# Kernel optimization log

Measured on AMD Instinct MI355X. Metric: run time of the kernel, lower is better.

The kernel has to match this reference:

```python
import jax, jax.numpy as jnp
import numpy as np

D_MODEL = 2048
N_HEADS = 16
HEAD_DIM = D_MODEL // N_HEADS
MLP_DIM = 4 * D_MODEL
RMS_EPS = 1e-6
MASK_VALUE = -1e9  # fp32 path in the original


def setup_inputs() -> dict:
    key = jax.random.key(0)
    ks = jax.random.split(key, 8)
    B, S = 2, 2048
    scale = 0.02
    return {
        "x": jax.random.normal(ks[0], (B, S, D_MODEL), dtype=jnp.float32),
        "attention_mask": jnp.ones((B, S), dtype=jnp.int32),
        "w_norm_attn": jnp.ones((D_MODEL,), dtype=jnp.float32),
        "wq": jax.random.normal(ks[1], (D_MODEL, D_MODEL), dtype=jnp.float32) * scale,
        "wk": jax.random.normal(ks[2], (D_MODEL, D_MODEL), dtype=jnp.float32) * scale,
        "wv": jax.random.normal(ks[3], (D_MODEL, D_MODEL), dtype=jnp.float32) * scale,
        "wo": jax.random.normal(ks[4], (D_MODEL, D_MODEL), dtype=jnp.float32) * scale,
        "w_norm_mlp": jnp.ones((D_MODEL,), dtype=jnp.float32),
        "w_up": jax.random.normal(ks[5], (MLP_DIM, D_MODEL), dtype=jnp.float32) * scale,
        "w_down": jax.random.normal(ks[6], (D_MODEL, MLP_DIM), dtype=jnp.float32) * scale,
    }


def _rmsnorm(x, w, eps=RMS_EPS):
    rms = jax.lax.rsqrt(jnp.mean(x * x, axis=-1, keepdims=True) + eps)
    return x * rms * w


def _split_heads(x):  # [B,S,D] -> [B,H,S,Dh]
    B, S, _ = x.shape
    return x.reshape(B, S, N_HEADS, HEAD_DIM).transpose(0, 2, 1, 3)


def reference(x, attention_mask, w_norm_attn, wq, wk, wv, wo, w_norm_mlp, w_up, w_down):
    B, S, _ = x.shape
    residual = x
    h = _rmsnorm(x, w_norm_attn)
    # nn.Linear(no bias): y = h @ W.T
    q = _split_heads(h @ wq.T)  # [B,H,S,Dh]
    k = _split_heads(h @ wk.T)
    v = _split_heads(h @ wv.T)

    scale = 1.0 / np.sqrt(HEAD_DIM)
    scores = jnp.einsum("bhqd,bhkd->bhqk", q, k) * scale  # [B,H,S,S]

    q_pos = jnp.arange(S)[:, None]
    k_pos = jnp.arange(S)[None, :]
    causal = k_pos <= q_pos  # [S,S]
    scores = jnp.where(causal[None, None], scores, MASK_VALUE)

    key_mask = attention_mask.astype(bool)  # [B,S]
    scores = jnp.where(key_mask[:, None, None, :], scores, MASK_VALUE)

    probs = jax.nn.softmax(scores.astype(jnp.float32), axis=-1).astype(q.dtype)
    probs = jnp.nan_to_num(probs, nan=0.0, posinf=0.0, neginf=0.0)

    att = jnp.einsum("bhqk,bhkd->bhqd", probs, v)  # [B,H,S,Dh]
    att = att.transpose(0, 2, 1, 3).reshape(B, S, D_MODEL)
    x = residual + att @ wo.T

    residual = x
    h = _rmsnorm(x, w_norm_mlp)
    h = jax.nn.gelu(h @ w_up.T, approximate=False)  # F.gelu default is exact erf
    x = residual + h @ w_down.T
    return x
```

## Files before the change

kernel.cpp:

```cpp
#include <hip/hip_runtime.h>

typedef unsigned short u16;
typedef __bf16 bf16x8 __attribute__((ext_vector_type(8)));
typedef float f32x4 __attribute__((ext_vector_type(4)));

#define SEQ 2048
#define DM 2048
#define NH 16
#define DHD 128
#define MLPD 8192
#define ATT_SCALE 0.08838834764831845f

__device__ __forceinline__ float bf2f(u16 u) {
  union { unsigned int i; float f; } c; c.i = ((unsigned int)u) << 16; return c.f;
}
__device__ __forceinline__ u16 f2bf(float f) {
  union { float f; unsigned int i; } c; c.f = f;
  unsigned int u = c.i;
  u += 0x7FFFu + ((u >> 16) & 1u);
  return (u16)(u >> 16);
}

__device__ __forceinline__ bool path_is_bf16(const unsigned* chk) {
  return chk[0] == 0x3F803F80u;
}

__device__ __forceinline__ void gl_lds16(const void* g, void* l) {
  __builtin_amdgcn_global_load_lds(
      (const __attribute__((address_space(1))) void*)g,
      (__attribute__((address_space(3))) void*)l, 16, 0, 0);
}

__global__ __launch_bounds__(256) void conv_w(const float* __restrict__ in,
                                              u16* __restrict__ out,
                                              const unsigned* __restrict__ chk) {
  if (path_is_bf16(chk)) return;
  size_t i = ((size_t)blockIdx.x * 256 + threadIdx.x) * 8;
  float4 a = *(const float4*)(in + i), b = *(const float4*)(in + i + 4);
  union { uint4 u; u16 s[8]; } o;
  o.s[0]=f2bf(a.x); o.s[1]=f2bf(a.y); o.s[2]=f2bf(a.z); o.s[3]=f2bf(a.w);
  o.s[4]=f2bf(b.x); o.s[5]=f2bf(b.y); o.s[6]=f2bf(b.z); o.s[7]=f2bf(b.w);
  *(uint4*)(out + i) = o.u;
}

template <typename TIN>
__global__ __launch_bounds__(256) void rms_x(const TIN* __restrict__ in,
                                             const TIN* __restrict__ wn,
                                             u16* __restrict__ out,
                                             const unsigned* __restrict__ chk,
                                             unsigned want) {
  if ((path_is_bf16(chk) ? 1u : 0u) != want) return;
  const int row = blockIdx.x;
  const int t = threadIdx.x;
  float f[8], wv[8];
  if constexpr (sizeof(TIN) == 4) {
    const float* p = (const float*)in + (size_t)row * DM + t * 8;
    float4 a = *(const float4*)p, b = *(const float4*)(p + 4);
    f[0]=a.x; f[1]=a.y; f[2]=a.z; f[3]=a.w; f[4]=b.x; f[5]=b.y; f[6]=b.z; f[7]=b.w;
    const float* wp = (const float*)wn + t * 8;
    float4 c = *(const float4*)wp, d = *(const float4*)(wp + 4);
    wv[0]=c.x; wv[1]=c.y; wv[2]=c.z; wv[3]=c.w; wv[4]=d.x; wv[5]=d.y; wv[6]=d.z; wv[7]=d.w;
  } else {
    union { uint4 u; u16 s[8]; } v;
    v.u = *(const uint4*)((const u16*)in + (size_t)row * DM + t * 8);
    union { uint4 u; u16 s[8]; } wu;
    wu.u = *(const uint4*)((const u16*)wn + t * 8);
#pragma unroll
    for (int i = 0; i < 8; i++) { f[i] = bf2f(v.s[i]); wv[i] = bf2f(wu.s[i]); }
  }
  float ss = 0.f;
#pragma unroll
  for (int i = 0; i < 8; i++) ss += f[i] * f[i];
#pragma unroll
  for (int off = 32; off >= 1; off >>= 1) ss += __shfl_xor(ss, off, 64);
  __shared__ float ws4[4];
  if ((t & 63) == 0) ws4[t >> 6] = ss;
  __syncthreads();
  float tot = ws4[0] + ws4[1] + ws4[2] + ws4[3];
  float rms = rsqrtf(tot * (1.0f / DM) + 1e-6f);
  union { uint4 u; u16 s[8]; } o;
#pragma unroll
  for (int i = 0; i < 8; i++) o.s[i] = f2bf(f[i] * rms * wv[i]);
  *(uint4*)(out + (size_t)row * DM + t * 8) = o.u;
}

template <int EPI, typename TB, typename TC>
__global__ __launch_bounds__(256, 2) void gemm_x(const u16* __restrict__ A,
                                                 const TB* __restrict__ B,
                                                 TC* __restrict__ C,
                                                 const TC* __restrict__ res,
                                                 int N, int K,
                                                 int Ald, int Bld, int Cld,
                                                 const unsigned* __restrict__ chk,
                                                 unsigned want) {
  if ((path_is_bf16(chk) ? 1u : 0u) != want) return;
  __shared__ u16 lA[128 * 32];
  __shared__ u16 lB[128 * 32];
  const int t = threadIdx.x;
  const int lane = t & 63;
  const int w = t >> 6;
  const int x = lane & 15;
  const int qd = lane >> 4;
  const int wr = w >> 1, wc = w & 1;
  const int m0 = blockIdx.y * 128, n0 = blockIdx.x * 128;

  const int c0 = t, c1 = t + 256;
  const u16* gA0 = A + (size_t)(m0 + (c0 >> 2)) * Ald + (c0 & 3) * 8;
  const u16* gA1 = A + (size_t)(m0 + (c1 >> 2)) * Ald + (c1 & 3) * 8;
  const TB* gB0 = B + (size_t)(n0 + (c0 >> 2)) * Bld + (c0 & 3) * 8;
  const TB* gB1 = B + (size_t)(n0 + (c1 >> 2)) * Bld + (c1 & 3) * 8;
  u16* sA0 = lA + c0 * 8; u16* sA1 = lA + c1 * 8;
  u16* sB0 = lB + c0 * 8; u16* sB1 = lB + c1 * 8;

  const u16* aAddr[4]; const u16* bAddr[4];
#pragma unroll
  for (int i = 0; i < 4; i++) {
    aAddr[i] = lA + (wr * 64 + i * 16 + x) * 32 + qd * 8;
    bAddr[i] = lB + (wc * 64 + i * 16 + x) * 32 + qd * 8;
  }

  const f32x4 ZV = {0.f, 0.f, 0.f, 0.f};
  f32x4 acc[4][4];
#pragma unroll
  for (int i = 0; i < 4; i++)
#pragma unroll
    for (int j = 0; j < 4; j++) acc[i][j] = ZV;

  for (int kk = 0; kk < K; kk += 32) {
    gl_lds16(gA0, sA0); gl_lds16(gA1, sA1);
    if constexpr (sizeof(TB) == 2) {
      gl_lds16(gB0, sB0); gl_lds16(gB1, sB1);
    } else {
      float4 a0 = *(const float4*)gB0, a1 = *(const float4*)(gB0 + 4);
      float4 b0 = *(const float4*)gB1, b1 = *(const float4*)(gB1 + 4);
      union { uint4 u; u16 s[8]; } p0, p1;
      p0.s[0]=f2bf(a0.x); p0.s[1]=f2bf(a0.y); p0.s[2]=f2bf(a0.z); p0.s[3]=f2bf(a0.w);
      p0.s[4]=f2bf(a1.x); p0.s[5]=f2bf(a1.y); p0.s[6]=f2bf(a1.z); p0.s[7]=f2bf(a1.w);
      p1.s[0]=f2bf(b0.x); p1.s[1]=f2bf(b0.y); p1.s[2]=f2bf(b0.z); p1.s[3]=f2bf(b0.w);
      p1.s[4]=f2bf(b1.x); p1.s[5]=f2bf(b1.y); p1.s[6]=f2bf(b1.z); p1.s[7]=f2bf(b1.w);
      *(uint4*)sB0 = p0.u;
      *(uint4*)sB1 = p1.u;
    }
    gA0 += 32; gA1 += 32; gB0 += 32; gB1 += 32;
    __syncthreads();
    bf16x8 aF[4], bF[4];
#pragma unroll
    for (int i = 0; i < 4; i++) {
      aF[i] = *(const bf16x8*)aAddr[i];
      bF[i] = *(const bf16x8*)bAddr[i];
    }
#pragma unroll
    for (int i = 0; i < 4; i++)
#pragma unroll
      for (int j = 0; j < 4; j++)
        acc[i][j] = __builtin_amdgcn_mfma_f32_16x16x32_bf16(aF[i], bF[j], acc[i][j], 0, 0, 0);
    __syncthreads();
  }

#pragma unroll
  for (int i = 0; i < 4; i++) {
    const int rg = m0 + wr * 64 + i * 16 + qd * 4;
#pragma unroll
    for (int j = 0; j < 4; j++) {
      const int cg = n0 + wc * 64 + j * 16 + x;
#pragma unroll
      for (int r = 0; r < 4; r++) {
        float v = acc[i][j][r];
        size_t idx = (size_t)(rg + r) * Cld + cg;
        if (EPI == 1) {
          if constexpr (sizeof(TC) == 4) v += ((const float*)res)[idx];
          else v += bf2f(((const u16*)res)[idx]);
        } else if (EPI == 2) {
          v = 0.5f * v * (1.0f + erff(v * 0.70710678118654752f));
        }
        if constexpr (sizeof(TC) == 4) ((float*)C)[idx] = v;
        else ((u16*)C)[idx] = f2bf(v);
      }
    }
  }
}

__global__ __launch_bounds__(256, 2) void attn_kernel(const u16* __restrict__ Q,
                                                      const u16* __restrict__ Kb,
                                                      const u16* __restrict__ V,
                                                      const int* __restrict__ mask,
                                                      u16* __restrict__ O) {
  __shared__ u16 lK[64 * 136];
  __shared__ u16 lV[128 * 72];
  __shared__ u16 lP[4 * 32 * 72];
  __shared__ float lBias[64];

  const int t = threadIdx.x;
  const int lane = t & 63;
  const int w = t >> 6;
  const int x = lane & 15;
  const int qd = lane >> 4;
  const int qt = blockIdx.x;
  const int b = blockIdx.y >> 4;
  const int h = blockIdx.y & 15;
  const int q0 = qt * 128 + w * 32;
  const size_t batchRow = (size_t)b * SEQ;

  bf16x8 qF[2][4];
#pragma unroll
  for (int mt = 0; mt < 2; mt++)
#pragma unroll
    for (int kf = 0; kf < 4; kf++)
      qF[mt][kf] = *(const bf16x8*)(Q + (batchRow + q0 + mt * 16 + x) * DM +
                                    h * DHD + kf * 32 + qd * 8);

  const f32x4 ZV = {0.f, 0.f, 0.f, 0.f};
  f32x4 oAcc[2][8];
#pragma unroll
  for (int mt = 0; mt < 2; mt++)
#pragma unroll
    for (int dt = 0; dt < 8; dt++) oAcc[mt][dt] = ZV;
  float mrow[2][4], lrow[2][4];
#pragma unroll
  for (int mt = 0; mt < 2; mt++)
#pragma unroll
    for (int r = 0; r < 4; r++) { mrow[mt][r] = -1e30f; lrow[mt][r] = 0.f; }

  const int nkt = min(SEQ / 64, 2 * qt + 2);
  u16* lPw = lP + w * (32 * 72);

  for (int kt = 0; kt < nkt; kt++) {
    const int k0 = kt * 64;
#pragma unroll
    for (int ii = 0; ii < 4; ii++) {
      int c = ii * 256 + t;
      int kr = c >> 4, ko = (c & 15) * 8;
      uint4 kvv = *(const uint4*)(Kb + (batchRow + k0 + kr) * DM + h * DHD + ko);
      *(uint4*)(lK + kr * 136 + ko) = kvv;
      union { uint4 u; u16 s[8]; } vv;
      vv.u = *(const uint4*)(V + (batchRow + k0 + kr) * DM + h * DHD + ko);
#pragma unroll
      for (int i = 0; i < 8; i++) lV[(ko + i) * 72 + kr] = vv.s[i];
    }
    if (t < 64) lBias[t] = mask[b * SEQ + k0 + t] ? 0.f : -1e9f;
    __syncthreads();

    f32x4 sAcc[2][4];
#pragma unroll
    for (int mt = 0; mt < 2; mt++)
#pragma unroll
      for (int nt = 0; nt < 4; nt++) sAcc[mt][nt] = ZV;
#pragma unroll
    for (int nt = 0; nt < 4; nt++) {
      bf16x8 kB[4];
#pragma unroll
      for (int kf = 0; kf < 4; kf++)
        kB[kf] = *(const bf16x8*)(lK + (nt * 16 + x) * 136 + kf * 32 + qd * 8);
#pragma unroll
      for (int mt = 0; mt < 2; mt++)
#pragma unroll
        for (int kf = 0; kf < 4; kf++)
          sAcc[mt][nt] = __builtin_amdgcn_mfma_f32_16x16x32_bf16(qF[mt][kf], kB[kf], sAcc[mt][nt], 0, 0, 0);
    }

#pragma unroll
    for (int mt = 0; mt < 2; mt++) {
#pragma unroll
      for (int r = 0; r < 4; r++) {
        const int qg = q0 + mt * 16 + qd * 4 + r;
        float sv[4]; float mx = -1e30f;
#pragma unroll
        for (int nt = 0; nt < 4; nt++) {
          int kg = k0 + nt * 16 + x;
          float s = sAcc[mt][nt][r] * ATT_SCALE + lBias[nt * 16 + x];
          if (kg > qg) s = -1e9f;
          sv[nt] = s;
          mx = fmaxf(mx, s);
        }
#pragma unroll
        for (int off = 1; off < 16; off <<= 1) mx = fmaxf(mx, __shfl_xor(mx, off, 16));
        const float mnew = fmaxf(mrow[mt][r], mx);
        const float alpha = __expf(mrow[mt][r] - mnew);
        mrow[mt][r] = mnew;
        float rs = 0.f;
#pragma unroll
        for (int nt = 0; nt < 4; nt++) {
          float p = __expf(sv[nt] - mnew);
          rs += p;
          lPw[(mt * 16 + qd * 4 + r) * 72 + nt * 16 + x] = f2bf(p);
        }
#pragma unroll
        for (int off = 1; off < 16; off <<= 1) rs += __shfl_xor(rs, off, 16);
        lrow[mt][r] = lrow[mt][r] * alpha + rs;
#pragma unroll
        for (int dt = 0; dt < 8; dt++) oAcc[mt][dt][r] *= alpha;
      }
    }
    __syncthreads();

#pragma unroll
    for (int kf2 = 0; kf2 < 2; kf2++) {
      bf16x8 aP[2];
#pragma unroll
      for (int mt = 0; mt < 2; mt++)
        aP[mt] = *(const bf16x8*)(lPw + (mt * 16 + x) * 72 + kf2 * 32 + qd * 8);
#pragma unroll
      for (int dt = 0; dt < 8; dt++) {
        bf16x8 vB = *(const bf16x8*)(lV + (dt * 16 + x) * 72 + kf2 * 32 + qd * 8);
#pragma unroll
        for (int mt = 0; mt < 2; mt++)
          oAcc[mt][dt] = __builtin_amdgcn_mfma_f32_16x16x32_bf16(aP[mt], vB, oAcc[mt][dt], 0, 0, 0);
      }
    }
    __syncthreads();
  }

#pragma unroll
  for (int mt = 0; mt < 2; mt++) {
    float inv[4];
#pragma unroll
    for (int r = 0; r < 4; r++) inv[r] = 1.f / lrow[mt][r];
#pragma unroll
    for (int dt = 0; dt < 8; dt++)
#pragma unroll
      for (int r = 0; r < 4; r++) {
        const int qg = q0 + mt * 16 + qd * 4 + r;
        O[(batchRow + qg) * DM + h * DHD + dt * 16 + x] = f2bf(oAcc[mt][dt][r] * inv[r]);
      }
  }
}

extern "C" void kernel_launch(void* const* d_in, const int* in_sizes, int n_in,
                              void* d_out, int out_size, void* d_ws, size_t ws_size,
                              hipStream_t stream) {
  (void)in_sizes; (void)n_in; (void)out_size;
  const int* mask = (const int*)d_in[1];
  const unsigned* chk = (const unsigned*)d_in[2];
  u16* ws = (u16*)d_ws;

  const size_t SZ = (size_t)4096 * DM;
  u16* hn  = ws + 0 * SZ;
  u16* q   = ws + 1 * SZ;
  u16* k   = ws + 2 * SZ;
  u16* v   = ws + 3 * SZ;
  u16* att = hn;
  u16* h2  = q;
  u16* g   = k;

  const size_t W2 = (size_t)DM * DM;
  const size_t WM = (size_t)MLPD * DM;
  u16* wb   = ws + 4 * SZ;
  u16* wqb  = wb;
  u16* wkb  = wb + 1 * W2;
  u16* wvb  = wb + 2 * W2;
  u16* wob  = wb + 3 * W2;
  u16* wupb = wb + 4 * W2;
  u16* wdnb = wb + 4 * W2 + WM;
  const size_t needed = (4 * SZ + 4 * W2 + 2 * WM) * sizeof(u16);
  const bool bigws = ws_size >= needed;

  const int M = 4096;
  const int MH = 4096;
  dim3 g2k(DM / 128, M / 128), gmh(MH / 128, M / 128);

  {
    const float* x   = (const float*)d_in[0];
    const float* wna = (const float*)d_in[2];
    const float* wq  = (const float*)d_in[3];
    const float* wk  = (const float*)d_in[4];
    const float* wv  = (const float*)d_in[5];
    if (bigws) {
      const float* wo  = (const float*)d_in[6];
      const float* wup = (const float*)d_in[8];
      const float* wdn = (const float*)d_in[9];
      conv_w<<<(int)(W2 / 2048), 256, 0, stream>>>(wq, wqb, chk);
      conv_w<<<(int)(W2 / 2048), 256, 0, stream>>>(wk, wkb, chk);
      conv_w<<<(int)(W2 / 2048), 256, 0, stream>>>(wv, wvb, chk);
      conv_w<<<(int)(W2 / 2048), 256, 0, stream>>>(wo, wob, chk);
      conv_w<<<(int)(WM / 2048), 256, 0, stream>>>(wup, wupb, chk);
      conv_w<<<(int)(WM / 2048), 256, 0, stream>>>(wdn, wdnb, chk);
    }
    rms_x<float><<<M, 256, 0, stream>>>(x, wna, hn, chk, 0);
    if (bigws) {
      gemm_x<0, u16, u16><<<g2k, 256, 0, stream>>>(hn, wqb, q, (u16*)nullptr, DM, DM, DM, DM, DM, chk, 0);
      gemm_x<0, u16, u16><<<g2k, 256, 0, stream>>>(hn, wkb, k, (u16*)nullptr, DM, DM, DM, DM, DM, chk, 0);
      gemm_x<0, u16, u16><<<g2k, 256, 0, stream>>>(hn, wvb, v, (u16*)nullptr, DM, DM, DM, DM, DM, chk, 0);
    } else {
      gemm_x<0, float, u16><<<g2k, 256, 0, stream>>>(hn, wq, q, (u16*)nullptr, DM, DM, DM, DM, DM, chk, 0);
      gemm_x<0, float, u16><<<g2k, 256, 0, stream>>>(hn, wk, k, (u16*)nullptr, DM, DM, DM, DM, DM, chk, 0);
      gemm_x<0, float, u16><<<g2k, 256, 0, stream>>>(hn, wv, v, (u16*)nullptr, DM, DM, DM, DM, DM, chk, 0);
    }
  }
  {
    const u16* x   = (const u16*)d_in[0];
    const u16* wna = (const u16*)d_in[2];
    const u16* wq  = (const u16*)d_in[3];
    const u16* wk  = (const u16*)d_in[4];
    const u16* wv  = (const u16*)d_in[5];
    rms_x<u16><<<M, 256, 0, stream>>>(x, wna, hn, chk, 1);
    gemm_x<0, u16, u16><<<g2k, 256, 0, stream>>>(hn, wq, q, (u16*)nullptr, DM, DM, DM, DM, DM, chk, 1);
    gemm_x<0, u16, u16><<<g2k, 256, 0, stream>>>(hn, wk, k, (u16*)nullptr, DM, DM, DM, DM, DM, chk, 1);
    gemm_x<0, u16, u16><<<g2k, 256, 0, stream>>>(hn, wv, v, (u16*)nullptr, DM, DM, DM, DM, DM, chk, 1);
  }

  attn_kernel<<<dim3(SEQ / 128, 32), 256, 0, stream>>>(q, k, v, mask, att);

  {
    const float* x   = (const float*)d_in[0];
    const float* wo  = (const float*)d_in[6];
    const float* wnm = (const float*)d_in[7];
    const float* wup = (const float*)d_in[8];
    const float* wdn = (const float*)d_in[9];
    float* out = (float*)d_out;
    if (bigws) {
      gemm_x<1, u16, float><<<g2k, 256, 0, stream>>>(att, wob, out, x, DM, DM, DM, DM, DM, chk, 0);
      rms_x<float><<<M, 256, 0, stream>>>(out, wnm, h2, chk, 0);
      gemm_x<2, u16, u16><<<gmh, 256, 0, stream>>>(h2, wupb, g, (u16*)nullptr, MH, DM, DM, DM, MH, chk, 0);
      gemm_x<1, u16, float><<<g2k, 256, 0, stream>>>(g, wdnb, out, out, DM, MH, MH, MLPD, DM, chk, 0);
      gemm_x<2, u16, u16><<<gmh, 256, 0, stream>>>(h2, wupb + (size_t)MH * DM, g, (u16*)nullptr, MH, DM, DM, DM, MH, chk, 0);
      gemm_x<1, u16, float><<<g2k, 256, 0, stream>>>(g, wdnb + MH, out, out, DM, MH, MH, MLPD, DM, chk, 0);
    } else {
      gemm_x<1, float, float><<<g2k, 256, 0, stream>>>(att, wo, out, x, DM, DM, DM, DM, DM, chk, 0);
      rms_x<float><<<M, 256, 0, stream>>>(out, wnm, h2, chk, 0);
      gemm_x<2, float, u16><<<gmh, 256, 0, stream>>>(h2, wup, g, (u16*)nullptr, MH, DM, DM, DM, MH, chk, 0);
      gemm_x<1, float, float><<<g2k, 256, 0, stream>>>(g, wdn, out, out, DM, MH, MH, MLPD, DM, chk, 0);
      gemm_x<2, float, u16><<<gmh, 256, 0, stream>>>(h2, wup + (size_t)MH * DM, g, (u16*)nullptr, MH, DM, DM, DM, MH, chk, 0);
      gemm_x<1, float, float><<<g2k, 256, 0, stream>>>(g, wdn + MH, out, out, DM, MH, MH, MLPD, DM, chk, 0);
    }
  }
  {
    const u16* x   = (const u16*)d_in[0];
    const u16* wo  = (const u16*)d_in[6];
    const u16* wnm = (const u16*)d_in[7];
    const u16* wup = (const u16*)d_in[8];
    const u16* wdn = (const u16*)d_in[9];
    u16* out = (u16*)d_out;
    gemm_x<1, u16, u16><<<g2k, 256, 0, stream>>>(att, wo, out, x, DM, DM, DM, DM, DM, chk, 1);
    rms_x<u16><<<M, 256, 0, stream>>>(out, wnm, h2, chk, 1);
    gemm_x<2, u16, u16><<<gmh, 256, 0, stream>>>(h2, wup, g, (u16*)nullptr, MH, DM, DM, DM, MH, chk, 1);
    gemm_x<1, u16, u16><<<g2k, 256, 0, stream>>>(g, wdn, out, out, DM, MH, MH, MLPD, DM, chk, 1);
    gemm_x<2, u16, u16><<<gmh, 256, 0, stream>>>(h2, wup + (size_t)MH * DM, g, (u16*)nullptr, MH, DM, DM, DM, MH, chk, 1);
    gemm_x<1, u16, u16><<<g2k, 256, 0, stream>>>(g, wdn + MH, out, out, DM, MH, MH, MLPD, DM, chk, 1);
  }
}
```

Measured before the change: 1.107 ms.

## Fuse QKV projections into one packed GEMM and trim attention syncs

Q, K and V are written into one packed buffer with row stride 6144. On the bf16-workspace path a single GEMM reads the contiguous wq/wk/wv converted weights to produce them, replacing three launches and improving grid fill. The attention kernel reads from the packed layout and keeps the key-mask bias in registers instead of LDS. It also drops the barrier between writing P and the PV MFMA, since each wave only reads its own P tile. The GEMM launch bound is raised to 3 waves per SIMD, and the P tile row padding is removed, which may add LDS bank conflicts.

```diff
diff --git a/kernel.cpp b/kernel.cpp
--- a/kernel.cpp
+++ b/kernel.cpp
@@ -9,6 +9,7 @@
 #define NH 16
 #define DHD 128
 #define MLPD 8192
+#define QKVLD 6144
 #define ATT_SCALE 0.08838834764831845f
 
 __device__ __forceinline__ float bf2f(u16 u) {
@@ -85,7 +86,7 @@
 }
 
 template <int EPI, typename TB, typename TC>
-__global__ __launch_bounds__(256, 2) void gemm_x(const u16* __restrict__ A,
+__global__ __launch_bounds__(256, 3) void gemm_x(const u16* __restrict__ A,
                                                  const TB* __restrict__ B,
                                                  TC* __restrict__ C,
                                                  const TC* __restrict__ res,
@@ -180,15 +181,12 @@
   }
 }
 
-__global__ __launch_bounds__(256, 2) void attn_kernel(const u16* __restrict__ Q,
-                                                      const u16* __restrict__ Kb,
-                                                      const u16* __restrict__ V,
+__global__ __launch_bounds__(256, 2) void attn_kernel(const u16* __restrict__ QKV,
                                                       const int* __restrict__ mask,
                                                       u16* __restrict__ O) {
   __shared__ u16 lK[64 * 136];
   __shared__ u16 lV[128 * 72];
-  __shared__ u16 lP[4 * 32 * 72];
-  __shared__ float lBias[64];
+  __shared__ u16 lP[4 * 32 * 64];
 
   const int t = threadIdx.x;
   const int lane = t & 63;
@@ -200,13 +198,16 @@
   const int h = blockIdx.y & 15;
   const int q0 = qt * 128 + w * 32;
   const size_t batchRow = (size_t)b * SEQ;
+  const u16* Q  = QKV;
+  const u16* Kb = QKV + 2048;
+  const u16* V  = QKV + 4096;
 
   bf16x8 qF[2][4];
 #pragma unroll
   for (int mt = 0; mt < 2; mt++)
 #pragma unroll
     for (int kf = 0; kf < 4; kf++)
-      qF[mt][kf] = *(const bf16x8*)(Q + (batchRow + q0 + mt * 16 + x) * DM +
+      qF[mt][kf] = *(const bf16x8*)(Q + (batchRow + q0 + mt * 16 + x) * QKVLD +
                                     h * DHD + kf * 32 + qd * 8);
 
   const f32x4 ZV = {0.f, 0.f, 0.f, 0.f};
@@ -222,7 +223,7 @@
     for (int r = 0; r < 4; r++) { mrow[mt][r] = -1e30f; lrow[mt][r] = 0.f; }
 
   const int nkt = min(SEQ / 64, 2 * qt + 2);
-  u16* lPw = lP + w * (32 * 72);
+  u16* lPw = lP + w * (32 * 64);
 
   for (int kt = 0; kt < nkt; kt++) {
     const int k0 = kt * 64;
@@ -230,14 +231,17 @@
     for (int ii = 0; ii < 4; ii++) {
       int c = ii * 256 + t;
       int kr = c >> 4, ko = (c & 15) * 8;
-      uint4 kvv = *(const uint4*)(Kb + (batchRow + k0 + kr) * DM + h * DHD + ko);
+      uint4 kvv = *(const uint4*)(Kb + (batchRow + k0 + kr) * QKVLD + h * DHD + ko);
       *(uint4*)(lK + kr * 136 + ko) = kvv;
       union { uint4 u; u16 s[8]; } vv;
-      vv.u = *(const uint4*)(V + (batchRow + k0 + kr) * DM + h * DHD + ko);
+      vv.u = *(const uint4*)(V + (batchRow + k0 + kr) * QKVLD + h * DHD + ko);
 #pragma unroll
       for (int i = 0; i < 8; i++) lV[(ko + i) * 72 + kr] = vv.s[i];
     }
-    if (t < 64) lBias[t] = mask[b * SEQ + k0 + t] ? 0.f : -1e9f;
+    float biasv[4];
+#pragma unroll
+    for (int nt = 0; nt < 4; nt++)
+      biasv[nt] = mask[b * SEQ + k0 + nt * 16 + x] ? 0.f : -1e9f;
     __syncthreads();
 
     f32x4 sAcc[2][4];
@@ -267,7 +271,7 @@
 #pragma unroll
         for (int nt = 0; nt < 4; nt++) {
           int kg = k0 + nt * 16 + x;
-          float s = sAcc[mt][nt][r] * ATT_SCALE + lBias[nt * 16 + x];
+          float s = sAcc[mt][nt][r] * ATT_SCALE + biasv[nt];
           if (kg > qg) s = -1e9f;
           sv[nt] = s;
           mx = fmaxf(mx, s);
@@ -282,7 +286,7 @@
         for (int nt = 0; nt < 4; nt++) {
           float p = __expf(sv[nt] - mnew);
           rs += p;
-          lPw[(mt * 16 + qd * 4 + r) * 72 + nt * 16 + x] = f2bf(p);
+          lPw[(mt * 16 + qd * 4 + r) * 64 + nt * 16 + x] = f2bf(p);
         }
 #pragma unroll
         for (int off = 1; off < 16; off <<= 1) rs += __shfl_xor(rs, off, 16);
@@ -291,14 +295,13 @@
         for (int dt = 0; dt < 8; dt++) oAcc[mt][dt][r] *= alpha;
       }
     }
-    __syncthreads();
 
 #pragma unroll
     for (int kf2 = 0; kf2 < 2; kf2++) {
       bf16x8 aP[2];
 #pragma unroll
       for (int mt = 0; mt < 2; mt++)
-        aP[mt] = *(const bf16x8*)(lPw + (mt * 16 + x) * 72 + kf2 * 32 + qd * 8);
+        aP[mt] = *(const bf16x8*)(lPw + (mt * 16 + x) * 64 + kf2 * 32 + qd * 8);
 #pragma unroll
       for (int dt = 0; dt < 8; dt++) {
         bf16x8 vB = *(const bf16x8*)(lV + (dt * 16 + x) * 72 + kf2 * 32 + qd * 8);
@@ -335,12 +338,10 @@
 
   const size_t SZ = (size_t)4096 * DM;
   u16* hn  = ws + 0 * SZ;
-  u16* q   = ws + 1 * SZ;
-  u16* k   = ws + 2 * SZ;
-  u16* v   = ws + 3 * SZ;
+  u16* pk  = ws + 1 * SZ;
   u16* att = hn;
-  u16* h2  = q;
-  u16* g   = k;
+  u16* h2  = pk;
+  u16* g   = ws + 2 * SZ;
 
   const size_t W2 = (size_t)DM * DM;
   const size_t WM = (size_t)MLPD * DM;
@@ -356,7 +357,7 @@
 
   const int M = 4096;
   const int MH = 4096;
-  dim3 g2k(DM / 128, M / 128), gmh(MH / 128, M / 128);
+  dim3 g2k(DM / 128, M / 128), gmh(MH / 128, M / 128), gqkv(QKVLD / 128, M / 128);
 
   {
     const float* x   = (const float*)d_in[0];
@@ -377,13 +378,11 @@
     }
     rms_x<float><<<M, 256, 0, stream>>>(x, wna, hn, chk, 0);
     if (bigws) {
-      gemm_x<0, u16, u16><<<g2k, 256, 0, stream>>>(hn, wqb, q, (u16*)nullptr, DM, DM, DM, DM, DM, chk, 0);
-      gemm_x<0, u16, u16><<<g2k, 256, 0, stream>>>(hn, wkb, k, (u16*)nullptr, DM, DM, DM, DM, DM, chk, 0);
-      gemm_x<0, u16, u16><<<g2k, 256, 0, stream>>>(hn, wvb, v, (u16*)nullptr, DM, DM, DM, DM, DM, chk, 0);
+      gemm_x<0, u16, u16><<<gqkv, 256, 0, stream>>>(hn, wqb, pk, (u16*)nullptr, QKVLD, DM, DM, DM, QKVLD, chk, 0);
     } else {
-      gemm_x<0, float, u16><<<g2k, 256, 0, stream>>>(hn, wq, q, (u16*)nullptr, DM, DM, DM, DM, DM, chk, 0);
-      gemm_x<0, float, u16><<<g2k, 256, 0, stream>>>(hn, wk, k, (u16*)nullptr, DM, DM, DM, DM, DM, chk, 0);
-      gemm_x<0, float, u16><<<g2k, 256, 0, stream>>>(hn, wv, v, (u16*)nullptr, DM, DM, DM, DM, DM, chk, 0);
+      gemm_x<0, float, u16><<<g2k, 256, 0, stream>>>(hn, wq, pk + 0,    (u16*)nullptr, DM, DM, DM, DM, QKVLD, chk, 0);
+      gemm_x<0, float, u16><<<g2k, 256, 0, stream>>>(hn, wk, pk + 2048, (u16*)nullptr, DM, DM, DM, DM, QKVLD, chk, 0);
+      gemm_x<0, float, u16><<<g2k, 256, 0, stream>>>(hn, wv, pk + 4096, (u16*)nullptr, DM, DM, DM, DM, QKVLD, chk, 0);
     }
   }
   {
@@ -393,12 +392,12 @@
     const u16* wk  = (const u16*)d_in[4];
     const u16* wv  = (const u16*)d_in[5];
     rms_x<u16><<<M, 256, 0, stream>>>(x, wna, hn, chk, 1);
-    gemm_x<0, u16, u16><<<g2k, 256, 0, stream>>>(hn, wq, q, (u16*)nullptr, DM, DM, DM, DM, DM, chk, 1);
-    gemm_x<0, u16, u16><<<g2k, 256, 0, stream>>>(hn, wk, k, (u16*)nullptr, DM, DM, DM, DM, DM, chk, 1);
-    gemm_x<0, u16, u16><<<g2k, 256, 0, stream>>>(hn, wv, v, (u16*)nullptr, DM, DM, DM, DM, DM, chk, 1);
-  }
-
-  attn_kernel<<<dim3(SEQ / 128, 32), 256, 0, stream>>>(q, k, v, mask, att);
+    gemm_x<0, u16, u16><<<g2k, 256, 0, stream>>>(hn, wq, pk + 0,    (u16*)nullptr, DM, DM, DM, DM, QKVLD, chk, 1);
+    gemm_x<0, u16, u16><<<g2k, 256, 0, stream>>>(hn, wk, pk + 2048, (u16*)nullptr, DM, DM, DM, DM, QKVLD, chk, 1);
+    gemm_x<0, u16, u16><<<g2k, 256, 0, stream>>>(hn, wv, pk + 4096, (u16*)nullptr, DM, DM, DM, DM, QKVLD, chk, 1);
+  }
+
+  attn_kernel<<<dim3(SEQ / 128, 32), 256, 0, stream>>>(pk, mask, att);
 
   {
     const float* x   = (const float*)d_in[0];
```

Result: faster. 1.075 ms (-3.0%).
